# Kernel tuning notes

Hardware: AMD Instinct MI355X
Metric: run time of the kernel (lower is better)

The kernel has to match this reference:

```python
import jax, jax.numpy as jnp
import numpy as np

H, KVH, D, R = 32, 8, 128, 32
MASK_OUT = 0.5
NEG = -1e9  # stand-in for finfo.min to avoid -inf accumulation; preserves ordering/softmax
ROPE_THETA = 10000.0


def _rope_tables(S, D):
    inv = 1.0 / (ROPE_THETA ** (np.arange(0, D, 2, dtype=np.float32) / D))
    t = np.arange(S, dtype=np.float32)
    freqs = np.outer(t, inv)
    emb = np.concatenate([freqs, freqs], axis=-1)  # [S, D]
    return jnp.asarray(np.cos(emb)), jnp.asarray(np.sin(emb))


def _apply_rope(x, cos, sin):
    # x: [B,H,S,D]; cos/sin: [S,D]
    x1, x2 = jnp.split(x, 2, axis=-1)
    rot = jnp.concatenate([-x2, x1], axis=-1)
    return x * cos[None, None] + rot * sin[None, None]


def setup_inputs() -> dict:
    B, S, E = 1, 1024, 4096
    key = jax.random.key(0)
    ks = jax.random.split(key, 9)
    n = lambda k, shp, sc=0.02: jax.random.normal(k, shp, jnp.float32) * sc
    return {
        'hidden_states': n(ks[0], (B, S, E), 1.0),
        'wq': n(ks[1], (E, H * D)),
        'wk': n(ks[2], (E, KVH * D)),
        'wv': n(ks[3], (E, KVH * D)),
        'wo': n(ks[4], (H * D, E)),
        'mixq': n(ks[5], (E, R)),
        'mixk': n(ks[6], (E, R)),
        'q_pos': n(ks[7], (S, H, R, D)),
        'k_pos': n(ks[8], (S, H, R, D)),
    }


def reference(hidden_states, wq, wk, wv, wo, mixq, mixk, q_pos, k_pos):
    B, S, E = hidden_states.shape
    rep = H // KVH
    # QKV projections -> [B, heads, S, D]
    q = (hidden_states @ wq).reshape(B, S, H, D).transpose(0, 2, 1, 3)
    k = (hidden_states @ wk).reshape(B, S, KVH, D).transpose(0, 2, 1, 3)
    v = (hidden_states @ wv).reshape(B, S, KVH, D).transpose(0, 2, 1, 3)
    k = jnp.repeat(k, rep, axis=1)  # repeat_kv (GQA expand) -> [B,H,S,D]
    v = jnp.repeat(v, rep, axis=1)

    cos, sin = _rope_tables(S, D)
    qr = _apply_rope(q, cos, sin)
    kr = _apply_rope(k, cos, sin)
    scale = 1.0 / jnp.sqrt(jnp.float32(D))
    true_score = jnp.einsum('bhqd,bhkd->bhqk', qr, kr) * scale  # [B,H,S,S]

    # low-rank position-dependent draft score
    lrq = hidden_states @ mixq  # [B,S,R]
    lrk = hidden_states @ mixk
    pq = jnp.einsum('bmr,mhrd->bhmd', lrq, q_pos)  # [B,H,S,D]
    pk = jnp.einsum('bnr,nhrd->bhnd', lrk, k_pos)
    draft_score = jnp.einsum('bhqd,bhkd->bhqk', pq, pk)  # [B,H,S,S]

    causal = jnp.where(jnp.tril(jnp.ones((S, S), dtype=bool)), 0.0, NEG).astype(jnp.float32)[None, None]
    draft_score = draft_score + causal  # prefill: add causal mask to draft score

    num_remain = S - int(S * MASK_OUT)
    _, draft_idx = jax.lax.top_k(draft_score, num_remain)  # [B,H,S,K]

    # scatter 0 at kept kv positions, NEG elsewhere
    bi = jnp.arange(B)[:, None, None, None]
    hi = jnp.arange(H)[None, :, None, None]
    qi = jnp.arange(S)[None, None, :, None]
    topk_mask = jnp.full((B, H, S, S), NEG, jnp.float32).at[bi, hi, qi, draft_idx].set(0.0)

    probs = jax.nn.softmax(true_score + causal + topk_mask, axis=-1)
    out = jnp.einsum('bhqk,bhkd->bqhd', probs, v).reshape(B, S, H * D)
    return out @ wo
```

## Files before the change

kernel.cpp:

```cpp
#include <hip/hip_runtime.h>
#include <hip/hip_bf16.h>
#include <math.h>


typedef unsigned short u16;
using bf16x8 = __attribute__((ext_vector_type(8))) short;
using f32x4  = __attribute__((ext_vector_type(4))) float;

#define NEGBIG -1e30f

__device__ __forceinline__ unsigned int fkey(float f) {
    unsigned int u = __float_as_uint(f);
    return (u & 0x80000000u) ? ~u : (u | 0x80000000u);
}

__device__ __forceinline__ u16 f2b(float f) {
    union { float f; unsigned u; } x; x.f = f;
    unsigned r = x.u + 0x7fffu + ((x.u >> 16) & 1u);
    return (u16)(r >> 16);
}

__device__ __forceinline__ void gl_lds16(const u16* g, u16* l) {
    __builtin_amdgcn_global_load_lds(
        (__attribute__((address_space(1))) void*)(g),
        (__attribute__((address_space(3))) void*)(l), 16, 0, 0);
}

__global__ __launch_bounds__(256) void init_kernel(
    const float* __restrict__ hs, u16* __restrict__ hs_bf,
    float* __restrict__ cosb, float* __restrict__ sinb)
{
    int bx = blockIdx.x, t = threadIdx.x;
    if (bx < 4096) {
        int i = bx * 256 + t;
        float4 v = ((const float4*)hs)[i];
        u16 o[4] = {f2b(v.x), f2b(v.y), f2b(v.z), f2b(v.w)};
        ((uint2*)hs_bf)[i] = *(const uint2*)o;
    } else {
        int row = (bx - 4096) * 4 + (t >> 6);
        int i = t & 63;
        double inv = pow(10000.0, -((double)(2 * i)) / 128.0);
        double ang = (double)row * inv;
        cosb[row * 64 + i] = (float)cos(ang);
        sinb[row * 64 + i] = (float)sin(ang);
    }
}

__device__ __forceinline__ void transpose_tile(
    const float* __restrict__ in, u16* __restrict__ out, int Kdim, int N,
    int bx, int by)
{
    __shared__ u16 tile[64][66];
    int n0 = bx * 64, k0 = by * 64;
    int t = threadIdx.x;
#pragma unroll
    for (int u = 0; u < 16; ++u) {
        int e = u * 256 + t; int r = e >> 6, c = e & 63;
        tile[r][c] = f2b(in[(size_t)(k0 + r) * N + n0 + c]);
    }
    __syncthreads();
#pragma unroll
    for (int u = 0; u < 16; ++u) {
        int e = u * 256 + t; int r = e >> 6, c = e & 63;
        out[(size_t)(n0 + r) * Kdim + k0 + c] = tile[c][r];
    }
}

__global__ __launch_bounds__(256) void transpose_bf16_kernel(
    const float* __restrict__ in, u16* __restrict__ out, int Kdim, int N)
{
    transpose_tile(in, out, Kdim, N, blockIdx.x, blockIdx.y);
}

__global__ __launch_bounds__(256) void transpose_qkvw_kernel(
    const float* __restrict__ wq, const float* __restrict__ wk, const float* __restrict__ wv,
    u16* __restrict__ wqT, u16* __restrict__ wkT, u16* __restrict__ wvT)
{
    int bx = blockIdx.x;
    const float* in; u16* outp; int N;
    if (bx < 64)      { in = wq; outp = wqT; N = 4096; }
    else if (bx < 80) { in = wk; outp = wkT; N = 1024; bx -= 64; }
    else              { in = wv; outp = wvT; N = 1024; bx -= 80; }
    transpose_tile(in, outp, 4096, N, bx, blockIdx.y);
}

__global__ __launch_bounds__(128) void rope_pack2_kernel(
    const float* __restrict__ qb, const float* __restrict__ kb,
    const float* __restrict__ cosb, const float* __restrict__ sinb,
    u16* __restrict__ qr, u16* __restrict__ kr)
{
    int s = blockIdx.x, h = blockIdx.y, d = threadIdx.x;
    const float* src; u16* dst; int W; float scale;
    if (h < 32) { src = qb; dst = qr; W = 4096; scale = 0.08838834764831845f; }
    else        { h -= 32; src = kb; dst = kr; W = 1024; scale = 1.0f; }
    float x  = src[(size_t)s * W + h * 128 + d];
    float x2 = src[(size_t)s * W + h * 128 + (d ^ 64)];
    float cs = cosb[s * 64 + (d & 63)];
    float sn = sinb[s * 64 + (d & 63)];
    float rot = (d < 64) ? -x2 : x2;
    dst[((size_t)h * 1024 + s) * 128 + d] = f2b((x * cs + rot * sn) * scale);
}

__device__ __forceinline__ void gemm_bf16_tile(
    const u16* __restrict__ A, const u16* __restrict__ BT, float* __restrict__ C,
    int Kdim, int Ncols, int bm, int bn)
{
    __shared__ u16 As[128 * 32];
    __shared__ u16 Bs[128 * 32];
    const int t = threadIdx.x;
    const int wave = t >> 6, lane = t & 63;
    const int wr = wave >> 1, wc = wave & 1;
    const int fr = lane & 15, fq = lane >> 4;

    f32x4 acc[4][4];
#pragma unroll
    for (int m = 0; m < 4; ++m)
#pragma unroll
        for (int n = 0; n < 4; ++n) acc[m][n] = 0.f;

    const int srow = 32 * wave + (lane >> 2);
    const int skc = (lane & 3) * 8;
    const u16* aS = A  + ((size_t)(bm * 128) + srow) * Kdim + skc;
    const u16* bS = BT + ((size_t)(bn * 128) + srow) * Kdim + skc;
    u16* aD0 = As + 1024 * wave;  u16* aD1 = aD0 + 512;
    u16* bD0 = Bs + 1024 * wave;  u16* bD1 = bD0 + 512;

    const int aoff = (wr * 64 + fr) * 32 + fq * 8;
    const int boff = (wc * 64 + fr) * 32 + fq * 8;

    for (int k0 = 0; k0 < Kdim; k0 += 32) {
        __syncthreads();
        gl_lds16(aS + k0, aD0);
        gl_lds16(aS + (size_t)16 * Kdim + k0, aD1);
        gl_lds16(bS + k0, bD0);
        gl_lds16(bS + (size_t)16 * Kdim + k0, bD1);
        __syncthreads();

        bf16x8 af[4], bfr[4];
#pragma unroll
        for (int m = 0; m < 4; ++m) af[m] = *(const bf16x8*)(As + aoff + m * 512);
#pragma unroll
        for (int n = 0; n < 4; ++n) bfr[n] = *(const bf16x8*)(Bs + boff + n * 512);
#pragma unroll
        for (int m = 0; m < 4; ++m)
#pragma unroll
            for (int n = 0; n < 4; ++n)
                acc[m][n] = __builtin_amdgcn_mfma_f32_16x16x32_bf16(af[m], bfr[n], acc[m][n], 0, 0, 0);
    }

    float* Cb = C + (size_t)(bm * 128 + wr * 64 + fq * 4) * Ncols + bn * 128 + wc * 64 + fr;
#pragma unroll
    for (int m = 0; m < 4; ++m)
#pragma unroll
        for (int j = 0; j < 4; ++j)
#pragma unroll
            for (int n = 0; n < 4; ++n)
                Cb[(size_t)(m * 16 + j) * Ncols + n * 16] = acc[m][n][j];
}

__global__ __launch_bounds__(256) void gemm_qkv_bf16_kernel(
    const u16* __restrict__ hs_bf, const u16* __restrict__ wqT,
    const u16* __restrict__ wkT, const u16* __restrict__ wvT,
    float* __restrict__ q, float* __restrict__ k, float* __restrict__ v)
{
    int bn = blockIdx.x, bm = blockIdx.y;
    const u16* Bsel; float* Csel; int Ncols;
    if (bn < 32)      { Bsel = wqT; Csel = q; Ncols = 4096; }
    else if (bn < 40) { Bsel = wkT; Csel = k; Ncols = 1024; bn -= 32; }
    else              { Bsel = wvT; Csel = v; Ncols = 1024; bn -= 40; }
    gemm_bf16_tile(hs_bf, Bsel, Csel, 4096, Ncols, bm, bn);
}

__global__ __launch_bounds__(256) void gemm_wo_bf16_kernel(
    const u16* __restrict__ attn_bf, const u16* __restrict__ woT, float* __restrict__ out)
{
    gemm_bf16_tile(attn_bf, woT, out, 4096, 4096, blockIdx.y, blockIdx.x);
}

__global__ __launch_bounds__(256) void lr_kernel(
    const float* __restrict__ hs, const float* __restrict__ mixq, const float* __restrict__ mixk,
    float* __restrict__ lrq, float* __restrict__ lrk)
{
    __shared__ float row[4096];
    __shared__ float part[2][32][4];
    int m = blockIdx.x, t = threadIdx.x;
#pragma unroll
    for (int u = 0; u < 4; ++u)
        ((float4*)row)[t + u * 256] = ((const float4*)(hs + (size_t)m * 4096))[t + u * 256];
    __syncthreads();
    int r = t & 31, which = (t >> 5) & 1, quarter = t >> 6;
    const float* mix = which ? mixk : mixq;
    float acc = 0.f;
    int kbase = quarter * 1024;
#pragma unroll 8
    for (int kk = 0; kk < 1024; ++kk)
        acc = fmaf(row[kbase + kk], mix[(size_t)(kbase + kk) * 32 + r], acc);
    part[which][r][quarter] = acc;
    __syncthreads();
    if (t < 64) {
        int r2 = t & 31, w2 = t >> 5;
        float s = part[w2][r2][0] + part[w2][r2][1] + part[w2][r2][2] + part[w2][r2][3];
        (w2 ? lrk : lrq)[(size_t)m * 32 + r2] = s;
    }
}

__global__ __launch_bounds__(128) void ppos2_kernel(
    const float* __restrict__ lrq, const float* __restrict__ lrk,
    const float* __restrict__ qpos, const float* __restrict__ kpos,
    float* __restrict__ pq, float* __restrict__ pk)
{
    int h = blockIdx.x, by = blockIdx.y, d = threadIdx.x;
    const float* lr; const float* pos; float* outp; int m;
    if (by < 512) { m = 512 + by; lr = lrq; pos = qpos; outp = pq; }
    else          { m = by - 512; lr = lrk; pos = kpos; outp = pk; }
    __shared__ float lrs[32];
    if (d < 32) lrs[d] = lr[(size_t)m * 32 + d];
    __syncthreads();
    const float* base = pos + ((size_t)(m * 32 + h) * 32) * 128 + d;
    float acc = 0.f;
#pragma unroll
    for (int r = 0; r < 32; ++r)
        acc = fmaf(lrs[r], base[(size_t)r * 128], acc);
    outp[((size_t)h * 1024 + m) * 128 + d] = acc;
}

__global__ __launch_bounds__(256) void draft_gemm_kernel(
    const float* __restrict__ pq, const float* __restrict__ pk,
    float* __restrict__ scores, int h0)
{
    int idx = blockIdx.x;
    int bm, bc;
    if (idx < 10)      { bm = 4; bc = idx; }
    else if (idx < 22) { bm = 5; bc = idx - 10; }
    else if (idx < 36) { bm = 6; bc = idx - 22; }
    else               { bm = 7; bc = idx - 36; }
    int hh = blockIdx.y;

    const float* A  = pq + ((size_t)(h0 + hh) * 1024 + bm * 128) * 128;
    const float* BT = pk + ((size_t)(h0 + hh) * 1024 + bc * 64) * 128;
    float* C = scores + ((size_t)hh * 512 + (bm - 4) * 128) * 1024 + bc * 64;

    __shared__ float As[8][128];
    __shared__ float Bs[8][64];
    const int t = threadIdx.x;
    const int tx = t & 15, ty = (t >> 4) & 15;

    float acc[8][4];
#pragma unroll
    for (int u = 0; u < 8; ++u)
#pragma unroll
        for (int w = 0; w < 4; ++w) acc[u][w] = 0.f;

    const int ai = t >> 1, ah = (t & 1) * 4;
    const int bi = t >> 2, bh = (t & 3) * 2;
    const float* Ap = A + (size_t)ai * 128 + ah;
    const float* Bp = BT + (size_t)bi * 128 + bh;

    for (int k0 = 0; k0 < 128; k0 += 8) {
        float4 av = *(const float4*)(Ap + k0);
        float2 bv = *(const float2*)(Bp + k0);
        __syncthreads();
        As[ah + 0][ai] = av.x; As[ah + 1][ai] = av.y;
        As[ah + 2][ai] = av.z; As[ah + 3][ai] = av.w;
        Bs[bh][bi] = bv.x; Bs[bh + 1][bi] = bv.y;
        __syncthreads();
#pragma unroll
        for (int kk = 0; kk < 8; ++kk) {
            float4 a0 = *(const float4*)(&As[kk][ty * 4]);
            float4 a1 = *(const float4*)(&As[kk][64 + ty * 4]);
            float4 b0 = *(const float4*)(&Bs[kk][tx * 4]);
            float aa[8] = {a0.x, a0.y, a0.z, a0.w, a1.x, a1.y, a1.z, a1.w};
#pragma unroll
            for (int u = 0; u < 8; ++u) {
                acc[u][0] = fmaf(aa[u], b0.x, acc[u][0]);
                acc[u][1] = fmaf(aa[u], b0.y, acc[u][1]);
                acc[u][2] = fmaf(aa[u], b0.z, acc[u][2]);
                acc[u][3] = fmaf(aa[u], b0.w, acc[u][3]);
            }
        }
    }
#pragma unroll
    for (int u = 0; u < 8; ++u) {
        int row = (u < 4) ? (ty * 4 + u) : (64 + ty * 4 + (u - 4));
        *(float4*)(C + (size_t)row * 1024 + tx * 4)
            = make_float4(acc[u][0], acc[u][1], acc[u][2], acc[u][3]);
    }
}

__global__ __launch_bounds__(256) void topk_select_kernel(
    const float* __restrict__ scores, int h0,
    unsigned long long* __restrict__ mask)
{
    int qt = blockIdx.x, hh = blockIdx.y;
    int h = h0 + hh;
    int t = threadIdx.x;
    const int i = t >> 4, jj = t & 15;
    const int lrow = qt * 16 + i;
    const int qrow = 512 + lrow;

    const float* src = scores + ((size_t)hh * 512 + lrow) * 1024;

    unsigned int vals[64];
#pragma unroll
    for (int g = 0; g < 16; ++g) {
        float4 v = *(const float4*)(src + g * 64 + jj * 4);
        int col = g * 64 + jj * 4;
        vals[g * 4 + 0] = fkey((col + 0) <= qrow ? v.x : NEGBIG);
        vals[g * 4 + 1] = fkey((col + 1) <= qrow ? v.y : NEGBIG);
        vals[g * 4 + 2] = fkey((col + 2) <= qrow ? v.z : NEGBIG);
        vals[g * 4 + 3] = fkey((col + 3) <= qrow ? v.w : NEGBIG);
    }

    unsigned int p = 0u;
    int kth = 512;
    for (int b = 31; b >= 0; --b) {
        unsigned int bit = 1u << b;
        unsigned int himask = (b == 31) ? 0u : (0xFFFFFFFFu << (b + 1));
        int cnt = 0;
#pragma unroll
        for (int n = 0; n < 64; ++n)
            cnt += (int)((((vals[n] ^ p) & himask) == 0u) && ((vals[n] & bit) != 0u));
        cnt += __shfl_xor(cnt, 1);
        cnt += __shfl_xor(cnt, 2);
        cnt += __shfl_xor(cnt, 4);
        cnt += __shfl_xor(cnt, 8);
        if (cnt >= kth) p |= bit; else kth -= cnt;
    }

    unsigned long long wpart[16];
#pragma unroll
    for (int w = 0; w < 16; ++w) wpart[w] = 0ull;
#pragma unroll
    for (int g = 0; g < 16; ++g)
#pragma unroll
        for (int e = 0; e < 4; ++e)
            wpart[g] |= ((unsigned long long)(vals[g * 4 + e] >= p)) << (4 * jj + e);
#pragma unroll
    for (int s = 1; s < 16; s <<= 1) {
#pragma unroll
        for (int w = 0; w < 16; ++w)
            wpart[w] |= __shfl_xor(wpart[w], s);
    }
    mask[((size_t)h * 1024 + qrow) * 16 + jj] = wpart[jj];
}

#define ATTN_KP 136
#define ATTN_VP 72

__global__ __launch_bounds__(256) void attn_mfma_kernel(
    const u16* __restrict__ qr, const u16* __restrict__ kr,
    const u16* __restrict__ vT,
    const unsigned long long* __restrict__ mask,
    u16* __restrict__ attn)
{
    int bx = blockIdx.x;
    int qt = (bx & 1) ? (bx >> 1) : (15 - (bx >> 1));
    int h = blockIdx.y;
    int kvh = h >> 2;
    int q0 = qt * 64;
    int t = threadIdx.x;
    int wave = t >> 6, lane = t & 63;
    int fr = lane & 15, fq = lane >> 4;
    int qrow = q0 + wave * 16 + fr;

    __shared__ u16 Ks[64 * ATTN_KP];
    __shared__ u16 Vs[128 * ATTN_VP];

    bf16x8 qf[4];
    const u16* qbase = qr + ((size_t)h * 1024 + qrow) * 128 + fq * 8;
#pragma unroll
    for (int kc = 0; kc < 4; ++kc)
        qf[kc] = *(const bf16x8*)(qbase + kc * 32);

    float m_run = -3.0e38f, l_run = 0.f;
    f32x4 accO[8];
#pragma unroll
    for (int m2 = 0; m2 < 8; ++m2) accO[m2] = 0.f;

    const unsigned long long* mrow = mask + ((size_t)h * 1024 + qrow) * 16;
    const bool use_mask = (qrow >= 512);
    const u16* kgh = kr + (size_t)kvh * 1024 * 128;
    const u16* vgh = vT + (size_t)kvh * 128 * 1024;

    int ntiles = qt + 1;
    for (int c = 0; c < ntiles; ++c) {
        int kv0 = c * 64;
        __syncthreads();
#pragma unroll
        for (int u = 0; u < 4; ++u) {
            int e = t + u * 256;
            int row = e >> 4, bc2 = (e & 15) * 8;
            uint4 d4 = *(const uint4*)(kgh + ((size_t)(kv0 + row)) * 128 + bc2);
            *(uint4*)(&Ks[row * ATTN_KP + bc2]) = d4;
        }
#pragma unroll
        for (int u = 0; u < 4; ++u) {
            int e = t + u * 256;
            int row = e >> 3, bc2 = (e & 7) * 8;
            uint4 d4 = *(const uint4*)(vgh + (size_t)row * 1024 + kv0 + bc2);
            *(uint4*)(&Vs[row * ATTN_VP + bc2]) = d4;
        }
        __syncthreads();

        f32x4 accS[4];
        accS[0] = 0.f; accS[1] = 0.f; accS[2] = 0.f; accS[3] = 0.f;
#pragma unroll
        for (int t2 = 0; t2 < 4; ++t2)
#pragma unroll
            for (int kc = 0; kc < 4; ++kc) {
                bf16x8 kf = *(const bf16x8*)(&Ks[(t2 * 16 + fr) * ATTN_KP + kc * 32 + fq * 8]);
                accS[t2] = __builtin_amdgcn_mfma_f32_16x16x32_bf16(kf, qf[kc], accS[t2], 0, 0, 0);
            }

        unsigned long long mw = use_mask ? mrow[c] : ~0ull;
        float p[4][4];
        float tmax = -3.0e38f;
#pragma unroll
        for (int t2 = 0; t2 < 4; ++t2)
#pragma unroll
            for (int j = 0; j < 4; ++j) {
                int kvi = (t2 << 4) + (fq << 2) + j;
                bool ok = ((mw >> kvi) & 1ull) && (kv0 + kvi <= qrow);
                float s = ok ? accS[t2][j] : -3.0e38f;
                p[t2][j] = s;
                tmax = fmaxf(tmax, s);
            }
        tmax = fmaxf(tmax, __shfl_xor(tmax, 16));
        tmax = fmaxf(tmax, __shfl_xor(tmax, 32));
        float m_new = fmaxf(m_run, tmax);
        float sf = __expf(m_run - m_new);
        float psum = 0.f;
#pragma unroll
        for (int t2 = 0; t2 < 4; ++t2)
#pragma unroll
            for (int j = 0; j < 4; ++j) {
                float e = (p[t2][j] > -1.0e38f) ? __expf(p[t2][j] - m_new) : 0.f;
                p[t2][j] = e;
                psum += e;
            }
        psum += __shfl_xor(psum, 16);
        psum += __shfl_xor(psum, 32);
        l_run = l_run * sf + psum;
        m_run = m_new;

#pragma unroll
        for (int m2 = 0; m2 < 8; ++m2) accO[m2] *= sf;

        union { uint4 u; bf16x8 b; } pc[2];
        int srcA = fr + ((fq & 1) << 5);
        int srcB = srcA + 16;
        bool hi = (fq & 2) != 0;
#pragma unroll
        for (int half = 0; half < 2; ++half) {
            unsigned W0, W1, W2, W3;
            asm("v_cvt_pk_bf16_f32 %0, %1, %2" : "=v"(W0) : "v"(p[2 * half][0]),     "v"(p[2 * half][1]));
            asm("v_cvt_pk_bf16_f32 %0, %1, %2" : "=v"(W1) : "v"(p[2 * half][2]),     "v"(p[2 * half][3]));
            asm("v_cvt_pk_bf16_f32 %0, %1, %2" : "=v"(W2) : "v"(p[2 * half + 1][0]), "v"(p[2 * half + 1][1]));
            asm("v_cvt_pk_bf16_f32 %0, %1, %2" : "=v"(W3) : "v"(p[2 * half + 1][2]), "v"(p[2 * half + 1][3]));
            unsigned a0 = __shfl(W0, srcA), a1 = __shfl(W1, srcA);
            unsigned a2 = __shfl(W2, srcA), a3 = __shfl(W3, srcA);
            unsigned b0 = __shfl(W0, srcB), b1 = __shfl(W1, srcB);
            unsigned b2 = __shfl(W2, srcB), b3 = __shfl(W3, srcB);
            pc[half].u.x = hi ? a2 : a0;
            pc[half].u.y = hi ? a3 : a1;
            pc[half].u.z = hi ? b2 : b0;
            pc[half].u.w = hi ? b3 : b1;
        }

#pragma unroll
        for (int m2 = 0; m2 < 8; ++m2) {
            bf16x8 vf0 = *(const bf16x8*)(&Vs[(m2 * 16 + fr) * ATTN_VP + fq * 8]);
            accO[m2] = __builtin_amdgcn_mfma_f32_16x16x32_bf16(vf0, pc[0].b, accO[m2], 0, 0, 0);
            bf16x8 vf1 = *(const bf16x8*)(&Vs[(m2 * 16 + fr) * ATTN_VP + 32 + fq * 8]);
            accO[m2] = __builtin_amdgcn_mfma_f32_16x16x32_bf16(vf1, pc[1].b, accO[m2], 0, 0, 0);
        }
    }

    float il = 1.0f / l_run;
    u16* obase = attn + (size_t)qrow * 4096 + h * 128 + fq * 4;
#pragma unroll
    for (int m2 = 0; m2 < 8; ++m2) {
        uint2 st;
        st.x = (unsigned)f2b(accO[m2][0] * il) | ((unsigned)f2b(accO[m2][1] * il) << 16);
        st.y = (unsigned)f2b(accO[m2][2] * il) | ((unsigned)f2b(accO[m2][3] * il) << 16);
        *(uint2*)(obase + m2 * 16) = st;
    }
}

extern "C" void kernel_launch(void* const* d_in, const int* in_sizes, int n_in,
                              void* d_out, int out_size, void* d_ws, size_t ws_size,
                              hipStream_t stream)
{
    (void)in_sizes; (void)n_in; (void)out_size; (void)ws_size;
    const float* hs   = (const float*)d_in[0];
    const float* wq   = (const float*)d_in[1];
    const float* wk   = (const float*)d_in[2];
    const float* wv   = (const float*)d_in[3];
    const float* wo   = (const float*)d_in[4];
    const float* mixq = (const float*)d_in[5];
    const float* mixk = (const float*)d_in[6];
    const float* qpos = (const float*)d_in[7];
    const float* kpos = (const float*)d_in[8];
    float* out = (float*)d_out;

    float* ws   = (float*)d_ws;
    float* qb   = ws;
    float* kb   = qb + 4194304;
    float* vb   = kb + 1048576;
    float* pq   = vb + 1048576;
    float* pk   = pq + 4194304;
    float* lrq  = pk + 4194304;
    float* lrk  = lrq + 32768;
    float* cosb = lrk + 32768;
    float* sinb = cosb + 65536;
    unsigned long long* mask = (unsigned long long*)(sinb + 65536);
    u16* hs_bf = (u16*)(ws + 14876672 + 1048576);
    u16* wkT   = hs_bf + 4194304;
    u16* wvT   = wkT + 4194304;
    u16* wqT   = (u16*)pq;
    u16* woT   = (u16*)pq;
    u16* qr_bf = (u16*)pq;
    u16* kr_bf = (u16*)pk;
    u16* vT_bf = (u16*)(pk + 1048576);
    u16* attn_bf = hs_bf;
    float* scores = (float*)hs_bf;

    hipLaunchKernelGGL(init_kernel, dim3(4352), dim3(256), 0, stream, hs, hs_bf, cosb, sinb);
    hipLaunchKernelGGL(transpose_qkvw_kernel, dim3(96, 64), dim3(256), 0, stream,
                       wq, wk, wv, wqT, wkT, wvT);
    hipLaunchKernelGGL(gemm_qkv_bf16_kernel, dim3(48, 8), dim3(256), 0, stream,
                       hs_bf, wqT, wkT, wvT, qb, kb, vb);
    hipLaunchKernelGGL(lr_kernel, dim3(1024), dim3(256), 0, stream, hs, mixq, mixk, lrq, lrk);
    hipLaunchKernelGGL(ppos2_kernel, dim3(32, 1536), dim3(128), 0, stream,
                       lrq, lrk, qpos, kpos, pq, pk);
    for (int h0 = 0; h0 < 32; h0 += 8) {
        hipLaunchKernelGGL(draft_gemm_kernel, dim3(52, 8), dim3(256), 0, stream,
                           pq, pk, scores, h0);
        hipLaunchKernelGGL(topk_select_kernel, dim3(32, 8), dim3(256), 0, stream,
                           scores, h0, mask);
    }
    hipLaunchKernelGGL(rope_pack2_kernel, dim3(1024, 40), dim3(128), 0, stream,
                       qb, kb, cosb, sinb, qr_bf, kr_bf);
    hipLaunchKernelGGL(transpose_bf16_kernel, dim3(16, 16), dim3(256), 0, stream, vb, vT_bf, 1024, 1024);
    hipLaunchKernelGGL(attn_mfma_kernel, dim3(16, 32), dim3(256), 0, stream,
                       qr_bf, kr_bf, vT_bf, mask, attn_bf);
    hipLaunchKernelGGL(transpose_bf16_kernel, dim3(64, 64), dim3(256), 0, stream, wo, woT, 4096, 4096);
    hipLaunchKernelGGL(gemm_wo_bf16_kernel, dim3(32, 8), dim3(256), 0, stream,
                       attn_bf, woT, out);
}
```

Measured before the change: 748.5 us.

## Split-K the QKV and Wo GEMMs, fuse init/lowrank/transpose and reduce-rope-V stages

Adds a large-workspace path that splits the QKV and output-projection GEMMs along K into two halves, doubling block count to fill more CUs. Partial sums are then combined in a reduction kernel that also applies RoPE and transposes V, or in a simple add kernel for the output. The bf16 conversion, rope tables, low-rank projection and weight transposes are merged into one launch, and draft/top-k run 16 heads per launch instead of 8. The cost is extra fp32 partial-result traffic and a dependence on a workspace of at least 123 MB, with the old path kept as a fallback.

```diff
diff --git a/kernel.cpp b/kernel.cpp
--- a/kernel.cpp
+++ b/kernel.cpp
@@ -4,10 +4,12 @@
 
 
 typedef unsigned short u16;
+typedef unsigned long long u64;
 using bf16x8 = __attribute__((ext_vector_type(8))) short;
 using f32x4  = __attribute__((ext_vector_type(4))) float;
 
 #define NEGBIG -1e30f
+#define QSCALE 0.08838834764831845f
 
 __device__ __forceinline__ unsigned int fkey(float f) {
     unsigned int u = __float_as_uint(f);
@@ -24,6 +26,15 @@
     __builtin_amdgcn_global_load_lds(
         (__attribute__((address_space(1))) void*)(g),
         (__attribute__((address_space(3))) void*)(l), 16, 0, 0);
+}
+
+__device__ __forceinline__ void rope_table_calc(int row, int i,
+    float* __restrict__ cosb, float* __restrict__ sinb)
+{
+    double inv = pow(10000.0, -((double)(2 * i)) / 128.0);
+    double ang = (double)row * inv;
+    cosb[row * 64 + i] = (float)cos(ang);
+    sinb[row * 64 + i] = (float)sin(ang);
 }
 
 __global__ __launch_bounds__(256) void init_kernel(
@@ -37,12 +48,7 @@
         u16 o[4] = {f2b(v.x), f2b(v.y), f2b(v.z), f2b(v.w)};
         ((uint2*)hs_bf)[i] = *(const uint2*)o;
     } else {
-        int row = (bx - 4096) * 4 + (t >> 6);
-        int i = t & 63;
-        double inv = pow(10000.0, -((double)(2 * i)) / 128.0);
-        double ang = (double)row * inv;
-        cosb[row * 64 + i] = (float)cos(ang);
-        sinb[row * 64 + i] = (float)sin(ang);
+        rope_table_calc((bx - 4096) * 4 + (t >> 6), t & 63, cosb, sinb);
     }
 }
 
@@ -84,6 +90,55 @@
     transpose_tile(in, outp, 4096, N, bx, blockIdx.y);
 }
 
+__global__ __launch_bounds__(256) void init_fused_kernel(
+    const float* __restrict__ hs, u16* __restrict__ hs_bf,
+    float* __restrict__ cosb, float* __restrict__ sinb,
+    const float* __restrict__ mixq, const float* __restrict__ mixk,
+    float* __restrict__ lrq, float* __restrict__ lrk,
+    const float* __restrict__ wq, const float* __restrict__ wk, const float* __restrict__ wv,
+    u16* __restrict__ wqT, u16* __restrict__ wkT, u16* __restrict__ wvT)
+{
+    __shared__ float row[4096];
+    __shared__ float part[2][32][4];
+    int bx = blockIdx.x, t = threadIdx.x;
+    if (bx < 4096) {
+        int i = bx * 256 + t;
+        float4 v = ((const float4*)hs)[i];
+        u16 o[4] = {f2b(v.x), f2b(v.y), f2b(v.z), f2b(v.w)};
+        ((uint2*)hs_bf)[i] = *(const uint2*)o;
+    } else if (bx < 4352) {
+        rope_table_calc((bx - 4096) * 4 + (t >> 6), t & 63, cosb, sinb);
+    } else if (bx < 5376) {
+        int m = bx - 4352;
+#pragma unroll
+        for (int u = 0; u < 4; ++u)
+            ((float4*)row)[t + u * 256] = ((const float4*)(hs + (size_t)m * 4096))[t + u * 256];
+        __syncthreads();
+        int r = t & 31, which = (t >> 5) & 1, quarter = t >> 6;
+        const float* mix = which ? mixk : mixq;
+        float acc = 0.f;
+        int kbase = quarter * 1024;
+#pragma unroll 8
+        for (int kk = 0; kk < 1024; ++kk)
+            acc = fmaf(row[kbase + kk], mix[(size_t)(kbase + kk) * 32 + r], acc);
+        part[which][r][quarter] = acc;
+        __syncthreads();
+        if (t < 64) {
+            int r2 = t & 31, w2 = t >> 5;
+            float s = part[w2][r2][0] + part[w2][r2][1] + part[w2][r2][2] + part[w2][r2][3];
+            (w2 ? lrk : lrq)[(size_t)m * 32 + r2] = s;
+        }
+    } else {
+        int idx = bx - 5376;
+        int bxT = idx % 96, byT = idx / 96;
+        const float* in; u16* outp; int N;
+        if (bxT < 64)      { in = wq; outp = wqT; N = 4096; }
+        else if (bxT < 80) { in = wk; outp = wkT; N = 1024; bxT -= 64; }
+        else               { in = wv; outp = wvT; N = 1024; bxT -= 80; }
+        transpose_tile(in, outp, 4096, N, bxT, byT);
+    }
+}
+
 __global__ __launch_bounds__(128) void rope_pack2_kernel(
     const float* __restrict__ qb, const float* __restrict__ kb,
     const float* __restrict__ cosb, const float* __restrict__ sinb,
@@ -91,7 +146,7 @@
 {
     int s = blockIdx.x, h = blockIdx.y, d = threadIdx.x;
     const float* src; u16* dst; int W; float scale;
-    if (h < 32) { src = qb; dst = qr; W = 4096; scale = 0.08838834764831845f; }
+    if (h < 32) { src = qb; dst = qr; W = 4096; scale = QSCALE; }
     else        { h -= 32; src = kb; dst = kr; W = 1024; scale = 1.0f; }
     float x  = src[(size_t)s * W + h * 128 + d];
     float x2 = src[(size_t)s * W + h * 128 + (d ^ 64)];
@@ -101,9 +156,59 @@
     dst[((size_t)h * 1024 + s) * 128 + d] = f2b((x * cs + rot * sn) * scale);
 }
 
-__device__ __forceinline__ void gemm_bf16_tile(
-    const u16* __restrict__ A, const u16* __restrict__ BT, float* __restrict__ C,
-    int Kdim, int Ncols, int bm, int bn)
+__global__ __launch_bounds__(256) void reduce_rope_v_kernel(
+    const float* __restrict__ C0, const float* __restrict__ C1,
+    const float* __restrict__ cosb, const float* __restrict__ sinb,
+    u16* __restrict__ qr, u16* __restrict__ kr, u16* __restrict__ vT)
+{
+    __shared__ u16 tile[64][66];
+    int bx = blockIdx.x, t = threadIdx.x;
+    if (bx < 20480) {
+        int sp = bx & 511, h40 = bx >> 9;
+        int s = sp * 2 + (t >> 7), d = t & 127;
+        int col; u16* dst; float scale;
+        if (h40 < 32) { col = h40 * 128 + d; dst = qr + ((size_t)h40 * 1024 + s) * 128 + d; scale = QSCALE; }
+        else { col = 4096 + (h40 - 32) * 128 + d; dst = kr + ((size_t)(h40 - 32) * 1024 + s) * 128 + d; scale = 1.0f; }
+        int colp = col ^ 64;
+        float x  = C0[(size_t)s * 6144 + col]  + C1[(size_t)s * 6144 + col];
+        float x2 = C0[(size_t)s * 6144 + colp] + C1[(size_t)s * 6144 + colp];
+        float cs = cosb[s * 64 + (d & 63)];
+        float sn = sinb[s * 64 + (d & 63)];
+        float rot = (d < 64) ? -x2 : x2;
+        *dst = f2b((x * cs + rot * sn) * scale);
+    } else {
+        int idx = bx - 20480;
+        int bxT = idx & 15, byT = idx >> 4;
+        int n0 = bxT * 64, k0 = byT * 64;
+#pragma unroll
+        for (int u = 0; u < 16; ++u) {
+            int e = u * 256 + t; int r = e >> 6, c = e & 63;
+            size_t off = (size_t)(k0 + r) * 6144 + 5120 + n0 + c;
+            tile[r][c] = f2b(C0[off] + C1[off]);
+        }
+        __syncthreads();
+#pragma unroll
+        for (int u = 0; u < 16; ++u) {
+            int e = u * 256 + t; int r = e >> 6, c = e & 63;
+            vT[(size_t)(n0 + r) * 1024 + k0 + c] = tile[c][r];
+        }
+    }
+}
+
+__global__ __launch_bounds__(256) void reduce_out_kernel(
+    const float* __restrict__ D0, const float* __restrict__ D1, float* __restrict__ out)
+{
+    int i = blockIdx.x * 256 + threadIdx.x;
+    float4 a = ((const float4*)D0)[i];
+    float4 b = ((const float4*)D1)[i];
+    ((float4*)out)[i] = make_float4(a.x + b.x, a.y + b.y, a.z + b.z, a.w + b.w);
+}
+
+__device__ __forceinline__ void gemm_bf16_panel(
+    const u16* __restrict__ Ap,
+    const u16* __restrict__ Bp,
+    float* __restrict__ Cp,
+    int Kdim, int kbase, int klen, int Cst)
 {
     __shared__ u16 As[128 * 32];
     __shared__ u16 Bs[128 * 32];
@@ -120,15 +225,15 @@
 
     const int srow = 32 * wave + (lane >> 2);
     const int skc = (lane & 3) * 8;
-    const u16* aS = A  + ((size_t)(bm * 128) + srow) * Kdim + skc;
-    const u16* bS = BT + ((size_t)(bn * 128) + srow) * Kdim + skc;
+    const u16* aS = Ap + (size_t)srow * Kdim + kbase + skc;
+    const u16* bS = Bp + (size_t)srow * Kdim + kbase + skc;
     u16* aD0 = As + 1024 * wave;  u16* aD1 = aD0 + 512;
     u16* bD0 = Bs + 1024 * wave;  u16* bD1 = bD0 + 512;
 
     const int aoff = (wr * 64 + fr) * 32 + fq * 8;
     const int boff = (wc * 64 + fr) * 32 + fq * 8;
 
-    for (int k0 = 0; k0 < Kdim; k0 += 32) {
+    for (int k0 = 0; k0 < klen; k0 += 32) {
         __syncthreads();
         gl_lds16(aS + k0, aD0);
         gl_lds16(aS + (size_t)16 * Kdim + k0, aD1);
@@ -148,14 +253,14 @@
                 acc[m][n] = __builtin_amdgcn_mfma_f32_16x16x32_bf16(af[m], bfr[n], acc[m][n], 0, 0, 0);
     }
 
-    float* Cb = C + (size_t)(bm * 128 + wr * 64 + fq * 4) * Ncols + bn * 128 + wc * 64 + fr;
+    float* Cb = Cp + (size_t)(wr * 64 + fq * 4) * Cst + wc * 64 + fr;
 #pragma unroll
     for (int m = 0; m < 4; ++m)
 #pragma unroll
         for (int j = 0; j < 4; ++j)
 #pragma unroll
             for (int n = 0; n < 4; ++n)
-                Cb[(size_t)(m * 16 + j) * Ncols + n * 16] = acc[m][n][j];
+                Cb[(size_t)(m * 16 + j) * Cst + n * 16] = acc[m][n][j];
 }
 
 __global__ __launch_bounds__(256) void gemm_qkv_bf16_kernel(
@@ -168,13 +273,41 @@
     if (bn < 32)      { Bsel = wqT; Csel = q; Ncols = 4096; }
     else if (bn < 40) { Bsel = wkT; Csel = k; Ncols = 1024; bn -= 32; }
     else              { Bsel = wvT; Csel = v; Ncols = 1024; bn -= 40; }
-    gemm_bf16_tile(hs_bf, Bsel, Csel, 4096, Ncols, bm, bn);
+    gemm_bf16_panel(hs_bf + (size_t)bm * 128 * 4096, Bsel + (size_t)bn * 128 * 4096,
+                    Csel + (size_t)bm * 128 * Ncols + bn * 128, 4096, 0, 4096, Ncols);
 }
 
 __global__ __launch_bounds__(256) void gemm_wo_bf16_kernel(
     const u16* __restrict__ attn_bf, const u16* __restrict__ woT, float* __restrict__ out)
 {
-    gemm_bf16_tile(attn_bf, woT, out, 4096, 4096, blockIdx.y, blockIdx.x);
+    int bn = blockIdx.x, bm = blockIdx.y;
+    gemm_bf16_panel(attn_bf + (size_t)bm * 128 * 4096, woT + (size_t)bn * 128 * 4096,
+                    out + (size_t)bm * 128 * 4096 + bn * 128, 4096, 0, 4096, 4096);
+}
+
+__global__ __launch_bounds__(256) void gemm_qkv_sk_kernel(
+    const u16* __restrict__ hs_bf, const u16* __restrict__ wqT,
+    const u16* __restrict__ wkT, const u16* __restrict__ wvT,
+    float* __restrict__ C0, float* __restrict__ C1)
+{
+    int bn = blockIdx.x, bm = blockIdx.y, g = blockIdx.z;
+    const u16* Bsel; int bnrow;
+    if (bn < 32)      { Bsel = wqT; bnrow = bn; }
+    else if (bn < 40) { Bsel = wkT; bnrow = bn - 32; }
+    else              { Bsel = wvT; bnrow = bn - 40; }
+    float* C = g ? C1 : C0;
+    gemm_bf16_panel(hs_bf + (size_t)bm * 128 * 4096, Bsel + (size_t)bnrow * 128 * 4096,
+                    C + (size_t)bm * 128 * 6144 + bn * 128, 4096, g * 2048, 2048, 6144);
+}
+
+__global__ __launch_bounds__(256) void gemm_wo_sk_kernel(
+    const u16* __restrict__ attn_bf, const u16* __restrict__ woT,
+    float* __restrict__ D0, float* __restrict__ D1)
+{
+    int bn = blockIdx.x, bm = blockIdx.y, g = blockIdx.z;
+    float* C = g ? D1 : D0;
+    gemm_bf16_panel(attn_bf + (size_t)bm * 128 * 4096, woT + (size_t)bn * 128 * 4096,
+                    C + (size_t)bm * 128 * 4096 + bn * 128, 4096, g * 2048, 2048, 4096);
 }
 
 __global__ __launch_bounds__(256) void lr_kernel(
@@ -491,7 +624,7 @@
                               void* d_out, int out_size, void* d_ws, size_t ws_size,
                               hipStream_t stream)
 {
-    (void)in_sizes; (void)n_in; (void)out_size; (void)ws_size;
+    (void)in_sizes; (void)n_in; (void)out_size;
     const float* hs   = (const float*)d_in[0];
     const float* wq   = (const float*)d_in[1];
     const float* wk   = (const float*)d_in[2];
@@ -502,49 +635,101 @@
     const float* qpos = (const float*)d_in[7];
     const float* kpos = (const float*)d_in[8];
     float* out = (float*)d_out;
-
-    float* ws   = (float*)d_ws;
-    float* qb   = ws;
-    float* kb   = qb + 4194304;
-    float* vb   = kb + 1048576;
-    float* pq   = vb + 1048576;
-    float* pk   = pq + 4194304;
-    float* lrq  = pk + 4194304;
-    float* lrk  = lrq + 32768;
-    float* cosb = lrk + 32768;
-    float* sinb = cosb + 65536;
-    unsigned long long* mask = (unsigned long long*)(sinb + 65536);
-    u16* hs_bf = (u16*)(ws + 14876672 + 1048576);
-    u16* wkT   = hs_bf + 4194304;
-    u16* wvT   = wkT + 4194304;
-    u16* wqT   = (u16*)pq;
-    u16* woT   = (u16*)pq;
-    u16* qr_bf = (u16*)pq;
-    u16* kr_bf = (u16*)pk;
-    u16* vT_bf = (u16*)(pk + 1048576);
-    u16* attn_bf = hs_bf;
-    float* scores = (float*)hs_bf;
-
-    hipLaunchKernelGGL(init_kernel, dim3(4352), dim3(256), 0, stream, hs, hs_bf, cosb, sinb);
-    hipLaunchKernelGGL(transpose_qkvw_kernel, dim3(96, 64), dim3(256), 0, stream,
-                       wq, wk, wv, wqT, wkT, wvT);
-    hipLaunchKernelGGL(gemm_qkv_bf16_kernel, dim3(48, 8), dim3(256), 0, stream,
-                       hs_bf, wqT, wkT, wvT, qb, kb, vb);
-    hipLaunchKernelGGL(lr_kernel, dim3(1024), dim3(256), 0, stream, hs, mixq, mixk, lrq, lrk);
-    hipLaunchKernelGGL(ppos2_kernel, dim3(32, 1536), dim3(128), 0, stream,
-                       lrq, lrk, qpos, kpos, pq, pk);
-    for (int h0 = 0; h0 < 32; h0 += 8) {
-        hipLaunchKernelGGL(draft_gemm_kernel, dim3(52, 8), dim3(256), 0, stream,
-                           pq, pk, scores, h0);
-        hipLaunchKernelGGL(topk_select_kernel, dim3(32, 8), dim3(256), 0, stream,
-                           scores, h0, mask);
-    }
-    hipLaunchKernelGGL(rope_pack2_kernel, dim3(1024, 40), dim3(128), 0, stream,
-                       qb, kb, cosb, sinb, qr_bf, kr_bf);
-    hipLaunchKernelGGL(transpose_bf16_kernel, dim3(16, 16), dim3(256), 0, stream, vb, vT_bf, 1024, 1024);
-    hipLaunchKernelGGL(attn_mfma_kernel, dim3(16, 32), dim3(256), 0, stream,
-                       qr_bf, kr_bf, vT_bf, mask, attn_bf);
-    hipLaunchKernelGGL(transpose_bf16_kernel, dim3(64, 64), dim3(256), 0, stream, wo, woT, 4096, 4096);
-    hipLaunchKernelGGL(gemm_wo_bf16_kernel, dim3(32, 8), dim3(256), 0, stream,
-                       attn_bf, woT, out);
-}
+    char* B = (char*)d_ws;
+    const size_t MB = 1ull << 20;
+
+    if (ws_size >= 123 * MB) {
+        u16* hs_bf = (u16*)(B);
+        u16* wkT   = (u16*)(B + 8 * MB);
+        u16* wvT   = (u16*)(B + 16 * MB);
+        u16* wqT   = (u16*)(B + 24 * MB);
+        u16* qr    = (u16*)(B + 24 * MB);
+        u16* kr    = (u16*)(B + 32 * MB);
+        u16* vT    = (u16*)(B + 34 * MB);
+        u16* woT   = (u16*)(B + 24 * MB);
+        float* C0  = (float*)(B + 56 * MB);
+        float* C1  = (float*)(B + 80 * MB);
+        float* pq  = (float*)(B + 56 * MB);
+        float* pk  = (float*)(B + 72 * MB);
+        float* scores = (float*)(B + 88 * MB);
+        float* D0  = (float*)(B + 56 * MB);
+        float* D1  = (float*)(B + 72 * MB);
+        u64* mask  = (u64*)(B + 120 * MB);
+        float* lrq = (float*)(B + 122 * MB);
+        float* lrk = lrq + 32768;
+        float* cosb = lrk + 32768;
+        float* sinb = cosb + 65536;
+        u16* attn_bf = hs_bf;
+
+        hipLaunchKernelGGL(init_fused_kernel, dim3(11520), dim3(256), 0, stream,
+                           hs, hs_bf, cosb, sinb, mixq, mixk, lrq, lrk,
+                           wq, wk, wv, wqT, wkT, wvT);
+        hipLaunchKernelGGL(gemm_qkv_sk_kernel, dim3(48, 8, 2), dim3(256), 0, stream,
+                           hs_bf, wqT, wkT, wvT, C0, C1);
+        hipLaunchKernelGGL(reduce_rope_v_kernel, dim3(20736), dim3(256), 0, stream,
+                           C0, C1, cosb, sinb, qr, kr, vT);
+        hipLaunchKernelGGL(ppos2_kernel, dim3(32, 1536), dim3(128), 0, stream,
+                           lrq, lrk, qpos, kpos, pq, pk);
+        for (int h0 = 0; h0 < 32; h0 += 16) {
+            hipLaunchKernelGGL(draft_gemm_kernel, dim3(52, 16), dim3(256), 0, stream,
+                               pq, pk, scores, h0);
+            hipLaunchKernelGGL(topk_select_kernel, dim3(32, 16), dim3(256), 0, stream,
+                               scores, h0, mask);
+        }
+        hipLaunchKernelGGL(attn_mfma_kernel, dim3(16, 32), dim3(256), 0, stream,
+                           qr, kr, vT, mask, attn_bf);
+        hipLaunchKernelGGL(transpose_bf16_kernel, dim3(64, 64), dim3(256), 0, stream,
+                           wo, woT, 4096, 4096);
+        hipLaunchKernelGGL(gemm_wo_sk_kernel, dim3(32, 8, 2), dim3(256), 0, stream,
+                           attn_bf, woT, D0, D1);
+        hipLaunchKernelGGL(reduce_out_kernel, dim3(4096), dim3(256), 0, stream,
+                           D0, D1, out);
+    } else {
+        float* ws   = (float*)d_ws;
+        float* qb   = ws;
+        float* kb   = qb + 4194304;
+        float* vb   = kb + 1048576;
+        float* pq   = vb + 1048576;
+        float* pk   = pq + 4194304;
+        float* lrq  = pk + 4194304;
+        float* lrk  = lrq + 32768;
+        float* cosb = lrk + 32768;
+        float* sinb = cosb + 65536;
+        u64* mask = (u64*)(sinb + 65536);
+        u16* hs_bf = (u16*)(ws + 14876672 + 1048576);
+        u16* wkT   = hs_bf + 4194304;
+        u16* wvT   = wkT + 4194304;
+        u16* wqT   = (u16*)pq;
+        u16* woT   = (u16*)pq;
+        u16* qr_bf = (u16*)pq;
+        u16* kr_bf = (u16*)pk;
+        u16* vT_bf = (u16*)(pk + 1048576);
+        u16* attn_bf = hs_bf;
+        float* scores = (float*)hs_bf;
+
+        hipLaunchKernelGGL(init_kernel, dim3(4352), dim3(256), 0, stream, hs, hs_bf, cosb, sinb);
+        hipLaunchKernelGGL(transpose_qkvw_kernel, dim3(96, 64), dim3(256), 0, stream,
+                           wq, wk, wv, wqT, wkT, wvT);
+        hipLaunchKernelGGL(gemm_qkv_bf16_kernel, dim3(48, 8), dim3(256), 0, stream,
+                           hs_bf, wqT, wkT, wvT, qb, kb, vb);
+        hipLaunchKernelGGL(lr_kernel, dim3(1024), dim3(256), 0, stream, hs, mixq, mixk, lrq, lrk);
+        hipLaunchKernelGGL(ppos2_kernel, dim3(32, 1536), dim3(128), 0, stream,
+                           lrq, lrk, qpos, kpos, pq, pk);
+        for (int h0 = 0; h0 < 32; h0 += 8) {
+            hipLaunchKernelGGL(draft_gemm_kernel, dim3(52, 8), dim3(256), 0, stream,
+                               pq, pk, scores, h0);
+            hipLaunchKernelGGL(topk_select_kernel, dim3(32, 8), dim3(256), 0, stream,
+                               scores, h0, mask);
+        }
+        hipLaunchKernelGGL(rope_pack2_kernel, dim3(1024, 40), dim3(128), 0, stream,
+                           qb, kb, cosb, sinb, qr_bf, kr_bf);
+        hipLaunchKernelGGL(transpose_bf16_kernel, dim3(16, 16), dim3(256), 0, stream,
+                           vb, vT_bf, 1024, 1024);
+        hipLaunchKernelGGL(attn_mfma_kernel, dim3(16, 32), dim3(256), 0, stream,
+                           qr_bf, kr_bf, vT_bf, mask, attn_bf);
+        hipLaunchKernelGGL(transpose_bf16_kernel, dim3(64, 64), dim3(256), 0, stream,
+                           wo, woT, 4096, 4096);
+        hipLaunchKernelGGL(gemm_wo_bf16_kernel, dim3(32, 8), dim3(256), 0, stream,
+                           attn_bf, woT, out);
+    }
+}
```

Measured after the change: 692.7 us. 1.08x faster.
